# Kernel tuning notes

Measured on AMD Instinct MI355X. Metric: run time of the kernel, lower is better.

The kernel has to match this reference:

```python
import jax, jax.numpy as jnp
import numpy as np

B, S, D, H = 2, 2048, 1024, 16
HD = D // H  # 64


def setup_inputs() -> dict:
    key = jax.random.key(0)
    ks = jax.random.split(key, 12)
    scale = 1.0 / np.sqrt(D)
    inp = {
        "input_query": jax.random.normal(ks[0], (B, S, D), jnp.float32),
        "input_key": jax.random.normal(ks[1], (B, S, D), jnp.float32),
        "input_value": jax.random.normal(ks[2], (B, S, D), jnp.float32),
        "mask": jax.random.randint(ks[3], (B, 1, S), 0, 2, jnp.int32),
        # torch nn.Linear params: y = x @ W.T + b, W shape (out, in)
        "wq": jax.random.uniform(ks[4], (D, D), jnp.float32, -scale, scale),
        "bq": jax.random.uniform(ks[5], (D,), jnp.float32, -scale, scale),
        "wk": jax.random.uniform(ks[6], (D, D), jnp.float32, -scale, scale),
        "bk": jax.random.uniform(ks[7], (D,), jnp.float32, -scale, scale),
        "wv": jax.random.uniform(ks[8], (D, D), jnp.float32, -scale, scale),
        "bv": jax.random.uniform(ks[9], (D,), jnp.float32, -scale, scale),
        "wo": jax.random.uniform(ks[10], (D, D), jnp.float32, -scale, scale),
        "bo": jax.random.uniform(ks[11], (D,), jnp.float32, -scale, scale),
    }
    return inp


def _split_heads(x):
    # (B, S, D) -> (B, H, S, HD)
    return x.reshape(B, S, H, HD).transpose(0, 2, 1, 3)


def reference(input_query, input_key, input_value, mask, wq, bq, wk, bk, wv, bv, wo, bo):
    q = _split_heads(input_query @ wq.T + bq)
    k = _split_heads(input_key @ wk.T + bk)
    v = _split_heads(input_value @ wv.T + bv)

    # scaled dot-product attention (materializes [B,H,S,S] as the original does)
    scores = jnp.einsum("bhqd,bhkd->bhqk", q, k) / np.sqrt(HD).astype(np.float32)
    # mask: (B, 1, S) -> unsqueeze(1) -> (B, 1, 1, S); fill -1e9 where mask == 0
    m = mask[:, None, :, :]
    scores = jnp.where(m == 0, jnp.float32(-1e9), scores)
    p_attn = jax.nn.softmax(scores, axis=-1)  # dropout is identity (rate 0 / eval)

    out = jnp.einsum("bhqk,bhkd->bhqd", p_attn, v)
    out = out.transpose(0, 2, 1, 3).reshape(B, S, D)
    return out @ wo.T + bo
```

## Files before the change

kernel.cpp:

```cpp
#include <hip/hip_runtime.h>
#include <math.h>

#define BB 2
#define SS 2048
#define DD 1024
#define HH 16
#define HD 64

typedef short short8 __attribute__((ext_vector_type(8)));
typedef float floatx4 __attribute__((ext_vector_type(4)));
typedef float floatx16 __attribute__((ext_vector_type(16)));
typedef unsigned int uintx2 __attribute__((ext_vector_type(2)));

__device__ inline ushort f2bf_rne(float x) {
    union { float f; unsigned u; } v; v.f = x;
    unsigned r = v.u + 0x7FFFu + ((v.u >> 16) & 1u);
    return (ushort)(r >> 16);
}
__device__ inline unsigned cvt_pk_bf16(float lo, float hi) {
    unsigned r;
    asm("v_cvt_pk_bf16_f32 %0, %1, %2" : "=v"(r) : "v"(lo), "v"(hi));
    return r;
}
__device__ inline short8 mk_pf(uintx2 x, uintx2 y) {
    union { unsigned u[4]; short8 s; } t;
    t.u[0] = x[0]; t.u[1] = y[0]; t.u[2] = x[1]; t.u[3] = y[1];
    return t.s;
}

#define GLD16(gp, lp) __builtin_amdgcn_global_load_lds( \
    (const __attribute__((address_space(1))) void*)(gp), \
    (__attribute__((address_space(3))) void*)(lp), 16, 0, 0)

__global__ __launch_bounds__(256)
void convert_bf16(const float* __restrict__ xq, const float* __restrict__ xk,
                  const float* __restrict__ xv,
                  const float* __restrict__ wq, const float* __restrict__ wk,
                  const float* __restrict__ wv, const float* __restrict__ wo,
                  ushort* __restrict__ Xq, ushort* __restrict__ Xk,
                  ushort* __restrict__ Xv,
                  ushort* __restrict__ Wq, ushort* __restrict__ Wk,
                  ushort* __restrict__ Wv, ushort* __restrict__ Wo)
{
    const int z = blockIdx.z;
    const size_t i = ((size_t)blockIdx.x * 256 + threadIdx.x) * 8;

    const float* src;
    ushort* dst;
    size_t off;
    if (z < 3) {
        src = (z == 0) ? xq : (z == 1) ? xk : xv;
        dst = (z == 0) ? Xq : (z == 1) ? Xk : Xv;
        off = i;
    } else {
        const int seg = (int)(i >> 20);
        off = i & ((1u << 20) - 1);
        src = (seg == 0) ? wq : (seg == 1) ? wk : (seg == 2) ? wv : wo;
        dst = (seg == 0) ? Wq : (seg == 1) ? Wk : (seg == 2) ? Wv : Wo;
    }
    float x[8];
    *(float4*)&x[0] = *(const float4*)(src + off);
    *(float4*)&x[4] = *(const float4*)(src + off + 4);
    short8 h8;
#pragma unroll
    for (int j = 0; j < 8; ++j) h8[j] = (short)f2bf_rne(x[j]);
    *(short8*)&dst[off] = h8;
}

__global__ __launch_bounds__(256, 3)
void qkv_gemm(const ushort* __restrict__ Xq, const ushort* __restrict__ Xk,
              const ushort* __restrict__ Xv,
              const ushort* __restrict__ Wq, const ushort* __restrict__ Wk,
              const ushort* __restrict__ Wv,
              const float* __restrict__ bq, const float* __restrict__ bk,
              const float* __restrict__ bv, const int* __restrict__ mask,
              ushort* __restrict__ Qo, ushort* __restrict__ Ko,
              ushort* __restrict__ Vo, float qscale)
{
    __shared__ __align__(16) ushort Alds[128][32];
    __shared__ __align__(16) ushort Blds[128][32];

    const int z   = blockIdx.z;
    const int tid = threadIdx.x;

    const ushort* X    = (z == 0) ? Xq : (z == 1) ? Xk : Xv;
    const ushort* W    = (z == 0) ? Wq : (z == 1) ? Wk : Wv;
    const float*  bias = (z == 0) ? bq : (z == 1) ? bk : bv;
    const float   osc  = (z == 0) ? qscale : 1.0f;

    const int lane = tid & 63;
    const int wave = tid >> 6;
    const int wr = wave >> 1;
    const int wc = wave & 1;
    const int lt = lane & 15;
    const int lq = lane >> 4;
    const int m0 = blockIdx.y * 128;
    const int n0 = blockIdx.x * 128;

    floatx4 acc[4][4];
#pragma unroll
    for (int mi = 0; mi < 4; ++mi)
#pragma unroll
        for (int ni = 0; ni < 4; ++ni) acc[mi][ni] = (floatx4)0.0f;

    const int srow = tid >> 2;
    const int sc   = (tid & 3) << 3;
    const ushort* gA0 = X + (size_t)(m0 + srow) * DD + sc;
    const ushort* gA1 = X + (size_t)(m0 + 64 + srow) * DD + sc;
    const ushort* gB0 = W + (size_t)(n0 + srow) * DD + sc;
    const ushort* gB1 = W + (size_t)(n0 + 64 + srow) * DD + sc;

    for (int k0 = 0; k0 < DD; k0 += 32) {
        __syncthreads();
        GLD16(gA0 + k0, &Alds[srow][sc]);
        GLD16(gA1 + k0, &Alds[64 + srow][sc]);
        GLD16(gB0 + k0, &Blds[srow][sc]);
        GLD16(gB1 + k0, &Blds[64 + srow][sc]);
        __syncthreads();

        short8 af[4], bf_[4];
#pragma unroll
        for (int mi = 0; mi < 4; ++mi)
            af[mi] = *(const short8*)&Alds[wr * 64 + mi * 16 + lt][lq * 8];
#pragma unroll
        for (int ni = 0; ni < 4; ++ni)
            bf_[ni] = *(const short8*)&Blds[wc * 64 + ni * 16 + lt][lq * 8];

#pragma unroll
        for (int mi = 0; mi < 4; ++mi)
#pragma unroll
            for (int ni = 0; ni < 4; ++ni)
                acc[mi][ni] = __builtin_amdgcn_mfma_f32_16x16x32_bf16(af[mi], bf_[ni], acc[mi][ni], 0, 0, 0);
    }

    float bbv[4];
#pragma unroll
    for (int ni = 0; ni < 4; ++ni) bbv[ni] = bias[n0 + wc * 64 + ni * 16 + lt];

    if (z == 2) {
#pragma unroll
        for (int mi = 0; mi < 4; ++mi) {
            const int mb  = m0 + wr * 64 + mi * 16 + lq * 4;
            const int bb_ = mb >> 11;
            const int s   = mb & (SS - 1);
            const int4 mm = *(const int4*)(mask + bb_ * SS + s);
            const float mf0 = (float)mm.x, mf1 = (float)mm.y;
            const float mf2 = (float)mm.z, mf3 = (float)mm.w;
#pragma unroll
            for (int ni = 0; ni < 4; ++ni) {
                const int n = n0 + wc * 64 + ni * 16 + lt;
                const int h = n >> 6;
                ushort4 pack;
                pack.x = f2bf_rne((acc[mi][ni][0] + bbv[ni]) * mf0);
                pack.y = f2bf_rne((acc[mi][ni][1] + bbv[ni]) * mf1);
                pack.z = f2bf_rne((acc[mi][ni][2] + bbv[ni]) * mf2);
                pack.w = f2bf_rne((acc[mi][ni][3] + bbv[ni]) * mf3);
                *(ushort4*)&Vo[(size_t)((bb_ * HH + h) * HD + (n & 63)) * SS + s] = pack;
            }
        }
    } else {
        ushort* C = z ? Ko : Qo;
#pragma unroll
        for (int mi = 0; mi < 4; ++mi) {
            const int mb  = m0 + wr * 64 + mi * 16 + lq * 4;
            const int bb_ = mb >> 11;
            const int s   = mb & (SS - 1);
            float mf[4] = {1.0f, 1.0f, 1.0f, 1.0f};
            if (z == 1) {
                const int4 mm = *(const int4*)(mask + bb_ * SS + s);
                mf[0] = (float)mm.x; mf[1] = (float)mm.y;
                mf[2] = (float)mm.z; mf[3] = (float)mm.w;
            }
#pragma unroll
            for (int ni = 0; ni < 4; ++ni) {
                const int n = n0 + wc * 64 + ni * 16 + lt;
                const int h = n >> 6;
#pragma unroll
                for (int r = 0; r < 4; ++r) {
                    C[(size_t)((bb_ * HH + h) * SS + (s + r)) * HD + (n & 63)] =
                        f2bf_rne((acc[mi][ni][r] + bbv[ni]) * osc * mf[r]);
                }
            }
        }
    }
}

#define LDV 68

__global__ __launch_bounds__(512, 4)
void attn_mfma(const ushort* __restrict__ Qb, const ushort* __restrict__ Kb,
               const ushort* __restrict__ Vt, const int* __restrict__ mask,
               ushort* __restrict__ Ob)
{
    __shared__ __align__(16) ushort KVlds[4][64][LDV];
    __shared__ int Wsum[8];

    const int tid  = threadIdx.x;
    const int lane = tid & 63;
    const int wave = tid >> 6;
    const int ll   = lane & 31;
    const int hi   = lane >> 5;
    const int qh   = wave & 3;
    const int ks   = wave >> 2;

    const int bid    = blockIdx.x;
    const int xcd    = bid & 7;
    const int slot   = bid >> 3;
    const int bhloc  = slot >> 4;
    const int qi     = slot & 15;
    const int bh     = xcd * 4 + bhloc;
    const int b      = bh >> 4;
    const int q0     = qi * 128;

    const size_t sbase = (size_t)bh * SS * HD;
    const size_t vbase = (size_t)bh * HD * SS;

    {
        const int4 ma = *(const int4*)(mask + b * SS + tid * 4);
        int s = ma.x + ma.y + ma.z + ma.w;
#pragma unroll
        for (int w = 32; w >= 1; w >>= 1) s += __shfl_xor(s, w);
        if (lane == 0) Wsum[wave] = s;
    }

    short8 ones;
#pragma unroll
    for (int j = 0; j < 8; ++j) ones[j] = (short)0x3F80;

    short8 qf[4];
    {
        const size_t qrow = sbase + (size_t)(q0 + qh * 32 + ll) * HD;
#pragma unroll
        for (int dc = 0; dc < 4; ++dc)
            qf[dc] = *(const short8*)(Qb + qrow + dc * 16 + hi * 8);
    }

    floatx16 oacc[2];
    oacc[0] = (floatx16)0.0f;
    oacc[1] = (floatx16)0.0f;
    floatx16 lacc = (floatx16)0.0f;

    const int srow = tid >> 3;
    const int sp8  = (tid & 7) << 3;

    short8 kr, vr;

    {
        kr = *(const short8*)(Kb + sbase + (size_t)srow * HD + sp8);
        vr = *(const short8*)(Vt + vbase + (size_t)srow * SS + sp8);
        *(short8*)&KVlds[0][srow][sp8] = kr;
        *(short8*)&KVlds[2][srow][sp8] = vr;
    }

    const int NT = SS / 64;
    for (int kt = 0; kt < NT; ++kt) {
        const int cur = kt & 1;
        __syncthreads();

        if (kt + 1 < NT) {
            const int k0n = (kt + 1) * 64;
            kr = *(const short8*)(Kb + sbase + (size_t)(k0n + srow) * HD + sp8);
            vr = *(const short8*)(Vt + vbase + (size_t)srow * SS + k0n + sp8);
        }

        short8 kf[4];
#pragma unroll
        for (int dc = 0; dc < 4; ++dc)
            kf[dc] = *(const short8*)&KVlds[cur][ks * 32 + ll][dc * 16 + hi * 8];

        floatx16 sacc = (floatx16)0.0f;
#pragma unroll
        for (int dc = 0; dc < 4; ++dc)
            sacc = __builtin_amdgcn_mfma_f32_32x32x16_bf16(kf[dc], qf[dc], sacc, 0, 0, 0);

        float p[16];
#pragma unroll
        for (int r = 0; r < 16; ++r) p[r] = __builtin_amdgcn_exp2f(sacc[r]);

        const unsigned pk_a = cvt_pk_bf16(p[0],  p[1]);
        const unsigned pk_b = cvt_pk_bf16(p[2],  p[3]);
        const unsigned pk_c = cvt_pk_bf16(p[4],  p[5]);
        const unsigned pk_d = cvt_pk_bf16(p[6],  p[7]);
        const unsigned pk_e = cvt_pk_bf16(p[8],  p[9]);
        const unsigned pk_f = cvt_pk_bf16(p[10], p[11]);
        const unsigned pk_g = cvt_pk_bf16(p[12], p[13]);
        const unsigned pk_h = cvt_pk_bf16(p[14], p[15]);
        const uintx2 s1 = __builtin_amdgcn_permlane32_swap(pk_a, pk_c, false, false);
        const uintx2 s2 = __builtin_amdgcn_permlane32_swap(pk_b, pk_d, false, false);
        const uintx2 s3 = __builtin_amdgcn_permlane32_swap(pk_e, pk_g, false, false);
        const uintx2 s4 = __builtin_amdgcn_permlane32_swap(pk_f, pk_h, false, false);
        const short8 pf0 = mk_pf(s1, s2);
        const short8 pf1 = mk_pf(s3, s4);

        lacc = __builtin_amdgcn_mfma_f32_32x32x16_bf16(pf0, ones, lacc, 0, 0, 0);
        lacc = __builtin_amdgcn_mfma_f32_32x32x16_bf16(pf1, ones, lacc, 0, 0, 0);

#pragma unroll
        for (int dn = 0; dn < 2; ++dn) {
            const short8 vf0 = *(const short8*)&KVlds[2 + cur][dn * 32 + ll][ks * 32 + hi * 8];
            const short8 vf1 = *(const short8*)&KVlds[2 + cur][dn * 32 + ll][ks * 32 + 16 + hi * 8];
            oacc[dn] = __builtin_amdgcn_mfma_f32_32x32x16_bf16(pf0, vf0, oacc[dn], 0, 0, 0);
            oacc[dn] = __builtin_amdgcn_mfma_f32_32x32x16_bf16(pf1, vf1, oacc[dn], 0, 0, 0);
        }

        if (kt + 1 < NT) {
            const int nxt = cur ^ 1;
            *(short8*)&KVlds[nxt][srow][sp8]     = kr;
            *(short8*)&KVlds[2 + nxt][srow][sp8] = vr;
        }
    }

    float* Cmb = (float*)&KVlds[0][0][0];
#pragma unroll
    for (int ph = 0; ph < 2; ++ph) {
        __syncthreads();
        if (ks == 1 && (qh >> 1) == ph) {
            const int sl = qh & 1;
#pragma unroll
            for (int dn = 0; dn < 2; ++dn)
#pragma unroll
                for (int r = 0; r < 16; ++r)
                    Cmb[((sl * 2 + dn) * 16 + r) * 64 + lane] = oacc[dn][r];
#pragma unroll
            for (int r = 0; r < 16; ++r)
                Cmb[4096 + (sl * 16 + r) * 64 + lane] = lacc[r];
        }
        __syncthreads();
        if (ks == 0 && (qh >> 1) == ph) {
            const int sl = qh & 1;
#pragma unroll
            for (int dn = 0; dn < 2; ++dn)
#pragma unroll
                for (int r = 0; r < 16; ++r)
                    oacc[dn][r] += Cmb[((sl * 2 + dn) * 16 + r) * 64 + lane];
#pragma unroll
            for (int r = 0; r < 16; ++r)
                lacc[r] += Cmb[4096 + (sl * 16 + r) * 64 + lane];
        }
    }

    if (ks == 0) {
        const int h = bh & 15;
        const float nmf = (float)(SS - (Wsum[0] + Wsum[1] + Wsum[2] + Wsum[3]
                                      + Wsum[4] + Wsum[5] + Wsum[6] + Wsum[7]));
        float linv[16];
#pragma unroll
        for (int r = 0; r < 16; ++r) linv[r] = 1.0f / (lacc[r] - nmf);
#pragma unroll
        for (int dn = 0; dn < 2; ++dn)
#pragma unroll
            for (int r = 0; r < 16; ++r) {
                const int q = q0 + qh * 32 + (r & 3) + 8 * (r >> 2) + 4 * hi;
                Ob[(size_t)(b * SS + q) * DD + h * HD + dn * 32 + ll] =
                    f2bf_rne(oacc[dn][r] * linv[r]);
            }
    }
}

__global__ __launch_bounds__(256, 3)
void o_gemm(const ushort* __restrict__ A, const ushort* __restrict__ B,
            const float* __restrict__ bias, float* __restrict__ out)
{
    __shared__ __align__(16) ushort sA[128][32];
    __shared__ __align__(16) ushort sB[128][32];

    const int tid  = threadIdx.x;
    const int lane = tid & 63;
    const int wave = tid >> 6;
    const int wr = wave >> 1;
    const int wc = wave & 1;
    const int lt = lane & 15;
    const int lq = lane >> 4;
    const int m0 = blockIdx.y * 128;
    const int n0 = blockIdx.x * 128;

    floatx4 acc[4][4];
#pragma unroll
    for (int mi = 0; mi < 4; ++mi)
#pragma unroll
        for (int ni = 0; ni < 4; ++ni) acc[mi][ni] = (floatx4)0.0f;

    const int srow = tid >> 2;
    const int sc   = (tid & 3) << 3;
    const ushort* gA0 = A + (size_t)(m0 + srow) * DD + sc;
    const ushort* gA1 = A + (size_t)(m0 + 64 + srow) * DD + sc;
    const ushort* gB0 = B + (size_t)(n0 + srow) * DD + sc;
    const ushort* gB1 = B + (size_t)(n0 + 64 + srow) * DD + sc;

    for (int k0 = 0; k0 < DD; k0 += 32) {
        __syncthreads();
        GLD16(gA0 + k0, &sA[srow][sc]);
        GLD16(gA1 + k0, &sA[64 + srow][sc]);
        GLD16(gB0 + k0, &sB[srow][sc]);
        GLD16(gB1 + k0, &sB[64 + srow][sc]);
        __syncthreads();

        short8 af[4], bf_[4];
#pragma unroll
        for (int mi = 0; mi < 4; ++mi)
            af[mi] = *(const short8*)&sA[wr * 64 + mi * 16 + lt][lq * 8];
#pragma unroll
        for (int ni = 0; ni < 4; ++ni)
            bf_[ni] = *(const short8*)&sB[wc * 64 + ni * 16 + lt][lq * 8];

#pragma unroll
        for (int mi = 0; mi < 4; ++mi)
#pragma unroll
            for (int ni = 0; ni < 4; ++ni)
                acc[mi][ni] = __builtin_amdgcn_mfma_f32_16x16x32_bf16(af[mi], bf_[ni], acc[mi][ni], 0, 0, 0);
    }

#pragma unroll
    for (int mi = 0; mi < 4; ++mi)
#pragma unroll
        for (int ni = 0; ni < 4; ++ni) {
            const int n = n0 + wc * 64 + ni * 16 + lt;
            const float bb = bias[n];
#pragma unroll
            for (int r = 0; r < 4; ++r) {
                const int m = m0 + wr * 64 + mi * 16 + lq * 4 + r;
                out[(size_t)m * DD + n] = acc[mi][ni][r] + bb;
            }
        }
}

extern "C" void kernel_launch(void* const* d_in, const int* in_sizes, int n_in,
                              void* d_out, int out_size, void* d_ws, size_t ws_size,
                              hipStream_t stream) {
    const float* xq   = (const float*)d_in[0];
    const float* xk   = (const float*)d_in[1];
    const float* xv   = (const float*)d_in[2];
    const int*   mask = (const int*)d_in[3];
    const float* wq   = (const float*)d_in[4];
    const float* bq   = (const float*)d_in[5];
    const float* wk   = (const float*)d_in[6];
    const float* bk   = (const float*)d_in[7];
    const float* wv   = (const float*)d_in[8];
    const float* bv   = (const float*)d_in[9];
    const float* wo   = (const float*)d_in[10];
    const float* bo   = (const float*)d_in[11];
    float* out = (float*)d_out;

    const size_t n = (size_t)BB * SS * DD;
    const size_t w1 = (size_t)DD * DD;

    ushort* Xqb = (ushort*)d_ws;
    ushort* Xkb = Xqb + n;
    ushort* Xvb = Xkb + n;
    ushort* Kb  = Xvb + n;
    ushort* Vt  = Kb + n;
    ushort* Wob = Vt + n;
    ushort* Ob  = Xqb;

    ushort* Qb  = (ushort*)out;
    ushort* Wqb = Qb + n;
    ushort* Wkb = Wqb + w1;
    ushort* Wvb = Wkb + w1;

    const float qscale = 0.125f * 1.44269504088896340736f;

    dim3 gc(2048, 1, 4);
    convert_bf16<<<gc, 256, 0, stream>>>(xq, xk, xv, wq, wk, wv, wo,
                                         Xqb, Xkb, Xvb, Wqb, Wkb, Wvb, Wob);

    dim3 g1(DD / 128, (BB * SS) / 128, 3);
    qkv_gemm<<<g1, 256, 0, stream>>>(Xqb, Xkb, Xvb, Wqb, Wkb, Wvb,
                                     bq, bk, bv, mask, Qb, Kb, Vt, qscale);

    attn_mfma<<<dim3(512), 512, 0, stream>>>(Qb, Kb, Vt, mask, Ob);

    dim3 g2(DD / 128, (BB * SS) / 128);
    o_gemm<<<g2, 256, 0, stream>>>(Ob, Wob, bo, out);
}
```

Baseline: 227.9 us.

## Stage QKV epilogue via LDS, shrink attention and output GEMM tiles

The QKV GEMM epilogue now writes results into a shared-memory staging buffer and then emits 16-byte coalesced stores to Q/K and transposed V, replacing scattered 2-byte and 8-byte stores. The attention kernel moves from 512-thread blocks over 128 queries to 256-thread blocks over 64 queries, doubling the grid. It also adds s_setprio around the MFMA bursts and simplifies the cross-wave reduction. The output GEMM uses 128x64 tiles so twice as many blocks cover the CUs, at the cost of less B-tile reuse and extra syncs in the epilogue.

```diff
diff --git a/kernel.cpp b/kernel.cpp
--- a/kernel.cpp
+++ b/kernel.cpp
@@ -77,8 +77,10 @@
               ushort* __restrict__ Qo, ushort* __restrict__ Ko,
               ushort* __restrict__ Vo, float qscale)
 {
-    __shared__ __align__(16) ushort Alds[128][32];
-    __shared__ __align__(16) ushort Blds[128][32];
+    __shared__ __align__(16) ushort SMEM[8704];
+#define ALDS(r, c) SMEM[(r) * 32 + (c)]
+#define BLDS(r, c) SMEM[4096 + (r) * 32 + (c)]
+#define EPI(r, c)  SMEM[(r) * 136 + (c)]
 
     const int z   = blockIdx.z;
     const int tid = threadIdx.x;
@@ -112,19 +114,19 @@
 
     for (int k0 = 0; k0 < DD; k0 += 32) {
         __syncthreads();
-        GLD16(gA0 + k0, &Alds[srow][sc]);
-        GLD16(gA1 + k0, &Alds[64 + srow][sc]);
-        GLD16(gB0 + k0, &Blds[srow][sc]);
-        GLD16(gB1 + k0, &Blds[64 + srow][sc]);
+        GLD16(gA0 + k0, &ALDS(srow, sc));
+        GLD16(gA1 + k0, &ALDS(64 + srow, sc));
+        GLD16(gB0 + k0, &BLDS(srow, sc));
+        GLD16(gB1 + k0, &BLDS(64 + srow, sc));
         __syncthreads();
 
         short8 af[4], bf_[4];
 #pragma unroll
         for (int mi = 0; mi < 4; ++mi)
-            af[mi] = *(const short8*)&Alds[wr * 64 + mi * 16 + lt][lq * 8];
+            af[mi] = *(const short8*)&ALDS(wr * 64 + mi * 16 + lt, lq * 8);
 #pragma unroll
         for (int ni = 0; ni < 4; ++ni)
-            bf_[ni] = *(const short8*)&Blds[wc * 64 + ni * 16 + lt][lq * 8];
+            bf_[ni] = *(const short8*)&BLDS(wc * 64 + ni * 16 + lt, lq * 8);
 
 #pragma unroll
         for (int mi = 0; mi < 4; ++mi)
@@ -139,85 +141,118 @@
 
     if (z == 2) {
 #pragma unroll
-        for (int mi = 0; mi < 4; ++mi) {
-            const int mb  = m0 + wr * 64 + mi * 16 + lq * 4;
-            const int bb_ = mb >> 11;
-            const int s   = mb & (SS - 1);
-            const int4 mm = *(const int4*)(mask + bb_ * SS + s);
-            const float mf0 = (float)mm.x, mf1 = (float)mm.y;
-            const float mf2 = (float)mm.z, mf3 = (float)mm.w;
-#pragma unroll
-            for (int ni = 0; ni < 4; ++ni) {
-                const int n = n0 + wc * 64 + ni * 16 + lt;
+        for (int half = 0; half < 2; ++half) {
+            __syncthreads();
+            if (wc == half) {
+#pragma unroll
+                for (int mi = 0; mi < 4; ++mi) {
+                    const int mb  = m0 + wr * 64 + mi * 16 + lq * 4;
+                    const int bb_ = mb >> 11;
+                    const int s   = mb & (SS - 1);
+                    const int4 mm = *(const int4*)(mask + bb_ * SS + s);
+                    const float mf[4] = {(float)mm.x, (float)mm.y, (float)mm.z, (float)mm.w};
+#pragma unroll
+                    for (int ni = 0; ni < 4; ++ni)
+#pragma unroll
+                        for (int r = 0; r < 4; ++r)
+                            EPI(ni * 16 + lt, wr * 64 + mi * 16 + lq * 4 + r) =
+                                f2bf_rne((acc[mi][ni][r] + bbv[ni]) * mf[r]);
+                }
+            }
+            __syncthreads();
+            const int b_ = m0 >> 11;
+            const int sB = m0 & (SS - 1);
+#pragma unroll
+            for (int u = 0; u < 4; ++u) {
+                const int idx = u * 256 + tid;
+                const int row = idx >> 4;
+                const int sg  = (idx & 15) << 3;
+                const short8 v = *(const short8*)&EPI(row, sg);
+                const int n = n0 + half * 64 + row;
                 const int h = n >> 6;
-                ushort4 pack;
-                pack.x = f2bf_rne((acc[mi][ni][0] + bbv[ni]) * mf0);
-                pack.y = f2bf_rne((acc[mi][ni][1] + bbv[ni]) * mf1);
-                pack.z = f2bf_rne((acc[mi][ni][2] + bbv[ni]) * mf2);
-                pack.w = f2bf_rne((acc[mi][ni][3] + bbv[ni]) * mf3);
-                *(ushort4*)&Vo[(size_t)((bb_ * HH + h) * HD + (n & 63)) * SS + s] = pack;
+                *(short8*)&Vo[((size_t)(b_ * HH + h) * HD + (n & 63)) * SS + sB + sg] = v;
             }
         }
     } else {
         ushort* C = z ? Ko : Qo;
 #pragma unroll
-        for (int mi = 0; mi < 4; ++mi) {
-            const int mb  = m0 + wr * 64 + mi * 16 + lq * 4;
-            const int bb_ = mb >> 11;
-            const int s   = mb & (SS - 1);
-            float mf[4] = {1.0f, 1.0f, 1.0f, 1.0f};
-            if (z == 1) {
-                const int4 mm = *(const int4*)(mask + bb_ * SS + s);
-                mf[0] = (float)mm.x; mf[1] = (float)mm.y;
-                mf[2] = (float)mm.z; mf[3] = (float)mm.w;
-            }
-#pragma unroll
-            for (int ni = 0; ni < 4; ++ni) {
-                const int n = n0 + wc * 64 + ni * 16 + lt;
-                const int h = n >> 6;
-#pragma unroll
-                for (int r = 0; r < 4; ++r) {
-                    C[(size_t)((bb_ * HH + h) * SS + (s + r)) * HD + (n & 63)] =
-                        f2bf_rne((acc[mi][ni][r] + bbv[ni]) * osc * mf[r]);
+        for (int half = 0; half < 2; ++half) {
+            __syncthreads();
+            if (wr == half) {
+#pragma unroll
+                for (int mi = 0; mi < 4; ++mi) {
+                    const int mb  = m0 + half * 64 + mi * 16 + lq * 4;
+                    const int bb_ = mb >> 11;
+                    const int s   = mb & (SS - 1);
+                    float mf[4] = {1.0f, 1.0f, 1.0f, 1.0f};
+                    if (z == 1) {
+                        const int4 mm = *(const int4*)(mask + bb_ * SS + s);
+                        mf[0] = (float)mm.x; mf[1] = (float)mm.y;
+                        mf[2] = (float)mm.z; mf[3] = (float)mm.w;
+                    }
+#pragma unroll
+                    for (int ni = 0; ni < 4; ++ni)
+#pragma unroll
+                        for (int r = 0; r < 4; ++r)
+                            EPI(mi * 16 + lq * 4 + r, wc * 64 + ni * 16 + lt) =
+                                f2bf_rne((acc[mi][ni][r] + bbv[ni]) * osc * mf[r]);
                 }
             }
+            __syncthreads();
+#pragma unroll
+            for (int u = 0; u < 4; ++u) {
+                const int idx = u * 256 + tid;
+                const int row = idx >> 4;
+                const int cg  = (idx & 15) << 3;
+                const short8 v = *(const short8*)&EPI(row, cg);
+                const int m = m0 + half * 64 + row;
+                const int n = n0 + cg;
+                const int h = n >> 6;
+                const int b_ = m >> 11;
+                const int s  = m & (SS - 1);
+                *(short8*)&C[((size_t)(b_ * HH + h) * SS + s) * HD + (n & 63)] = v;
+            }
         }
     }
+#undef ALDS
+#undef BLDS
+#undef EPI
 }
 
 #define LDV 68
 
-__global__ __launch_bounds__(512, 4)
+__global__ __launch_bounds__(256, 4)
 void attn_mfma(const ushort* __restrict__ Qb, const ushort* __restrict__ Kb,
                const ushort* __restrict__ Vt, const int* __restrict__ mask,
                ushort* __restrict__ Ob)
 {
     __shared__ __align__(16) ushort KVlds[4][64][LDV];
-    __shared__ int Wsum[8];
+    __shared__ int Wsum[4];
 
     const int tid  = threadIdx.x;
     const int lane = tid & 63;
     const int wave = tid >> 6;
     const int ll   = lane & 31;
     const int hi   = lane >> 5;
-    const int qh   = wave & 3;
-    const int ks   = wave >> 2;
+    const int qh   = wave & 1;
+    const int ks   = wave >> 1;
 
     const int bid    = blockIdx.x;
     const int xcd    = bid & 7;
     const int slot   = bid >> 3;
-    const int bhloc  = slot >> 4;
-    const int qi     = slot & 15;
+    const int bhloc  = slot >> 5;
+    const int qi     = slot & 31;
     const int bh     = xcd * 4 + bhloc;
     const int b      = bh >> 4;
-    const int q0     = qi * 128;
+    const int q0     = qi * 64;
 
     const size_t sbase = (size_t)bh * SS * HD;
     const size_t vbase = (size_t)bh * HD * SS;
 
     {
-        const int4 ma = *(const int4*)(mask + b * SS + tid * 4);
-        int s = ma.x + ma.y + ma.z + ma.w;
+        const int4 ma = *(const int4*)(mask + b * SS + tid * 8);
+        const int4 mb = *(const int4*)(mask + b * SS + tid * 8 + 4);
+        int s = ma.x + ma.y + ma.z + ma.w + mb.x + mb.y + mb.z + mb.w;
 #pragma unroll
         for (int w = 32; w >= 1; w >>= 1) s += __shfl_xor(s, w);
         if (lane == 0) Wsum[wave] = s;
@@ -240,16 +275,22 @@
     oacc[1] = (floatx16)0.0f;
     floatx16 lacc = (floatx16)0.0f;
 
-    const int srow = tid >> 3;
-    const int sp8  = (tid & 7) << 3;
-
-    short8 kr, vr;
+    const int srow = tid >> 2;
+    const int sp16 = (tid & 3) << 4;
+
+    short8 kr0, kr1, vr0, vr1;
 
     {
-        kr = *(const short8*)(Kb + sbase + (size_t)srow * HD + sp8);
-        vr = *(const short8*)(Vt + vbase + (size_t)srow * SS + sp8);
-        *(short8*)&KVlds[0][srow][sp8] = kr;
-        *(short8*)&KVlds[2][srow][sp8] = vr;
+        const size_t koff = sbase + (size_t)srow * HD + sp16;
+        kr0 = *(const short8*)(Kb + koff);
+        kr1 = *(const short8*)(Kb + koff + 8);
+        const size_t voff = vbase + (size_t)srow * SS + sp16;
+        vr0 = *(const short8*)(Vt + voff);
+        vr1 = *(const short8*)(Vt + voff + 8);
+        *(short8*)&KVlds[0][srow][sp16]     = kr0;
+        *(short8*)&KVlds[0][srow][sp16 + 8] = kr1;
+        *(short8*)&KVlds[2][srow][sp16]     = vr0;
+        *(short8*)&KVlds[2][srow][sp16 + 8] = vr1;
     }
 
     const int NT = SS / 64;
@@ -259,8 +300,12 @@
 
         if (kt + 1 < NT) {
             const int k0n = (kt + 1) * 64;
-            kr = *(const short8*)(Kb + sbase + (size_t)(k0n + srow) * HD + sp8);
-            vr = *(const short8*)(Vt + vbase + (size_t)srow * SS + k0n + sp8);
+            const size_t koff = sbase + (size_t)(k0n + srow) * HD + sp16;
+            kr0 = *(const short8*)(Kb + koff);
+            kr1 = *(const short8*)(Kb + koff + 8);
+            const size_t voff = vbase + (size_t)srow * SS + k0n + sp16;
+            vr0 = *(const short8*)(Vt + voff);
+            vr1 = *(const short8*)(Vt + voff + 8);
         }
 
         short8 kf[4];
@@ -269,9 +314,11 @@
             kf[dc] = *(const short8*)&KVlds[cur][ks * 32 + ll][dc * 16 + hi * 8];
 
         floatx16 sacc = (floatx16)0.0f;
+        __builtin_amdgcn_s_setprio(1);
 #pragma unroll
         for (int dc = 0; dc < 4; ++dc)
             sacc = __builtin_amdgcn_mfma_f32_32x32x16_bf16(kf[dc], qf[dc], sacc, 0, 0, 0);
+        __builtin_amdgcn_s_setprio(0);
 
         float p[16];
 #pragma unroll
@@ -292,9 +339,9 @@
         const short8 pf0 = mk_pf(s1, s2);
         const short8 pf1 = mk_pf(s3, s4);
 
+        __builtin_amdgcn_s_setprio(1);
         lacc = __builtin_amdgcn_mfma_f32_32x32x16_bf16(pf0, ones, lacc, 0, 0, 0);
         lacc = __builtin_amdgcn_mfma_f32_32x32x16_bf16(pf1, ones, lacc, 0, 0, 0);
-
 #pragma unroll
         for (int dn = 0; dn < 2; ++dn) {
             const short8 vf0 = *(const short8*)&KVlds[2 + cur][dn * 32 + ll][ks * 32 + hi * 8];
@@ -302,47 +349,42 @@
             oacc[dn] = __builtin_amdgcn_mfma_f32_32x32x16_bf16(pf0, vf0, oacc[dn], 0, 0, 0);
             oacc[dn] = __builtin_amdgcn_mfma_f32_32x32x16_bf16(pf1, vf1, oacc[dn], 0, 0, 0);
         }
+        __builtin_amdgcn_s_setprio(0);
 
         if (kt + 1 < NT) {
             const int nxt = cur ^ 1;
-            *(short8*)&KVlds[nxt][srow][sp8]     = kr;
-            *(short8*)&KVlds[2 + nxt][srow][sp8] = vr;
+            *(short8*)&KVlds[nxt][srow][sp16]     = kr0;
+            *(short8*)&KVlds[nxt][srow][sp16 + 8] = kr1;
+            *(short8*)&KVlds[2 + nxt][srow][sp16]     = vr0;
+            *(short8*)&KVlds[2 + nxt][srow][sp16 + 8] = vr1;
         }
     }
 
     float* Cmb = (float*)&KVlds[0][0][0];
-#pragma unroll
-    for (int ph = 0; ph < 2; ++ph) {
-        __syncthreads();
-        if (ks == 1 && (qh >> 1) == ph) {
-            const int sl = qh & 1;
-#pragma unroll
-            for (int dn = 0; dn < 2; ++dn)
-#pragma unroll
-                for (int r = 0; r < 16; ++r)
-                    Cmb[((sl * 2 + dn) * 16 + r) * 64 + lane] = oacc[dn][r];
+    __syncthreads();
+    if (ks == 1) {
+#pragma unroll
+        for (int dn = 0; dn < 2; ++dn)
 #pragma unroll
             for (int r = 0; r < 16; ++r)
-                Cmb[4096 + (sl * 16 + r) * 64 + lane] = lacc[r];
-        }
-        __syncthreads();
-        if (ks == 0 && (qh >> 1) == ph) {
-            const int sl = qh & 1;
-#pragma unroll
-            for (int dn = 0; dn < 2; ++dn)
-#pragma unroll
-                for (int r = 0; r < 16; ++r)
-                    oacc[dn][r] += Cmb[((sl * 2 + dn) * 16 + r) * 64 + lane];
+                Cmb[((qh * 2 + dn) * 16 + r) * 64 + lane] = oacc[dn][r];
+#pragma unroll
+        for (int r = 0; r < 16; ++r)
+            Cmb[4096 + (qh * 16 + r) * 64 + lane] = lacc[r];
+    }
+    __syncthreads();
+    if (ks == 0) {
+#pragma unroll
+        for (int dn = 0; dn < 2; ++dn)
 #pragma unroll
             for (int r = 0; r < 16; ++r)
-                lacc[r] += Cmb[4096 + (sl * 16 + r) * 64 + lane];
-        }
-    }
-
-    if (ks == 0) {
+                oacc[dn][r] += Cmb[((qh * 2 + dn) * 16 + r) * 64 + lane];
+#pragma unroll
+        for (int r = 0; r < 16; ++r)
+            lacc[r] += Cmb[4096 + (qh * 16 + r) * 64 + lane];
+
         const int h = bh & 15;
-        const float nmf = (float)(SS - (Wsum[0] + Wsum[1] + Wsum[2] + Wsum[3]
-                                      + Wsum[4] + Wsum[5] + Wsum[6] + Wsum[7]));
+        const float nmf = (float)(SS - (Wsum[0] + Wsum[1] + Wsum[2] + Wsum[3]));
         float linv[16];
 #pragma unroll
         for (int r = 0; r < 16; ++r) linv[r] = 1.0f / (lacc[r] - nmf);
@@ -362,7 +404,7 @@
             const float* __restrict__ bias, float* __restrict__ out)
 {
     __shared__ __align__(16) ushort sA[128][32];
-    __shared__ __align__(16) ushort sB[128][32];
+    __shared__ __align__(16) ushort sB[64][32];
 
     const int tid  = threadIdx.x;
     const int lane = tid & 63;
@@ -372,49 +414,47 @@
     const int lt = lane & 15;
     const int lq = lane >> 4;
     const int m0 = blockIdx.y * 128;
-    const int n0 = blockIdx.x * 128;
-
-    floatx4 acc[4][4];
+    const int n0 = blockIdx.x * 64;
+
+    floatx4 acc[4][2];
 #pragma unroll
     for (int mi = 0; mi < 4; ++mi)
 #pragma unroll
-        for (int ni = 0; ni < 4; ++ni) acc[mi][ni] = (floatx4)0.0f;
+        for (int ni = 0; ni < 2; ++ni) acc[mi][ni] = (floatx4)0.0f;
 
     const int srow = tid >> 2;
     const int sc   = (tid & 3) << 3;
     const ushort* gA0 = A + (size_t)(m0 + srow) * DD + sc;
     const ushort* gA1 = A + (size_t)(m0 + 64 + srow) * DD + sc;
     const ushort* gB0 = B + (size_t)(n0 + srow) * DD + sc;
-    const ushort* gB1 = B + (size_t)(n0 + 64 + srow) * DD + sc;
 
     for (int k0 = 0; k0 < DD; k0 += 32) {
         __syncthreads();
         GLD16(gA0 + k0, &sA[srow][sc]);
         GLD16(gA1 + k0, &sA[64 + srow][sc]);
         GLD16(gB0 + k0, &sB[srow][sc]);
-        GLD16(gB1 + k0, &sB[64 + srow][sc]);
         __syncthreads();
 
-        short8 af[4], bf_[4];
+        short8 af[4], bf_[2];
 #pragma unroll
         for (int mi = 0; mi < 4; ++mi)
             af[mi] = *(const short8*)&sA[wr * 64 + mi * 16 + lt][lq * 8];
 #pragma unroll
-        for (int ni = 0; ni < 4; ++ni)
-            bf_[ni] = *(const short8*)&sB[wc * 64 + ni * 16 + lt][lq * 8];
+        for (int ni = 0; ni < 2; ++ni)
+            bf_[ni] = *(const short8*)&sB[wc * 32 + ni * 16 + lt][lq * 8];
 
 #pragma unroll
         for (int mi = 0; mi < 4; ++mi)
 #pragma unroll
-            for (int ni = 0; ni < 4; ++ni)
+            for (int ni = 0; ni < 2; ++ni)
                 acc[mi][ni] = __builtin_amdgcn_mfma_f32_16x16x32_bf16(af[mi], bf_[ni], acc[mi][ni], 0, 0, 0);
     }
 
 #pragma unroll
     for (int mi = 0; mi < 4; ++mi)
 #pragma unroll
-        for (int ni = 0; ni < 4; ++ni) {
-            const int n = n0 + wc * 64 + ni * 16 + lt;
+        for (int ni = 0; ni < 2; ++ni) {
+            const int n = n0 + wc * 32 + ni * 16 + lt;
             const float bb = bias[n];
 #pragma unroll
             for (int r = 0; r < 4; ++r) {
@@ -467,8 +507,8 @@
     qkv_gemm<<<g1, 256, 0, stream>>>(Xqb, Xkb, Xvb, Wqb, Wkb, Wvb,
                                      bq, bk, bv, mask, Qb, Kb, Vt, qscale);
 
-    attn_mfma<<<dim3(512), 512, 0, stream>>>(Qb, Kb, Vt, mask, Ob);
-
-    dim3 g2(DD / 128, (BB * SS) / 128);
+    attn_mfma<<<dim3(1024), 256, 0, stream>>>(Qb, Kb, Vt, mask, Ob);
+
+    dim3 g2(DD / 64, (BB * SS) / 128);
     o_gemm<<<g2, 256, 0, stream>>>(Ob, Wob, bo, out);
 }
```

Measured after the change: 219.4 us. 3.7% less time.

## Fuse fp32-to-bf16 conversion into GEMM loads, remap blocks, add MFMA priorities

Applied to the files above, without the earlier changes.

Removes the separate conversion kernel. The QKV and output GEMMs now load fp32 activations and weights directly, convert them to bf16 in registers, and write them to LDS. Both GEMMs move to 1D grids with XCD-aware block remapping, and the output GEMM switches to 128x64 tiles so it launches more blocks. The attention loop wraps its MFMA sections in s_setprio. This saves a full read/write pass over the inputs and weights, but the GEMMs now read twice the bytes per tile through plain register loads instead of direct-to-LDS loads, and weights are re-converted by every block.

```diff
diff --git a/kernel.cpp b/kernel.cpp
--- a/kernel.cpp
+++ b/kernel.cpp
@@ -22,6 +22,14 @@
     asm("v_cvt_pk_bf16_f32 %0, %1, %2" : "=v"(r) : "v"(lo), "v"(hi));
     return r;
 }
+__device__ inline short8 cvt8(float4 lo, float4 hi) {
+    union { unsigned u[4]; short8 s; } t;
+    t.u[0] = cvt_pk_bf16(lo.x, lo.y);
+    t.u[1] = cvt_pk_bf16(lo.z, lo.w);
+    t.u[2] = cvt_pk_bf16(hi.x, hi.y);
+    t.u[3] = cvt_pk_bf16(hi.z, hi.w);
+    return t.s;
+}
 __device__ inline short8 mk_pf(uintx2 x, uintx2 y) {
     union { unsigned u[4]; short8 s; } t;
     t.u[0] = x[0]; t.u[1] = y[0]; t.u[2] = x[1]; t.u[3] = y[1];
@@ -32,46 +40,11 @@
     (const __attribute__((address_space(1))) void*)(gp), \
     (__attribute__((address_space(3))) void*)(lp), 16, 0, 0)
 
-__global__ __launch_bounds__(256)
-void convert_bf16(const float* __restrict__ xq, const float* __restrict__ xk,
-                  const float* __restrict__ xv,
-                  const float* __restrict__ wq, const float* __restrict__ wk,
-                  const float* __restrict__ wv, const float* __restrict__ wo,
-                  ushort* __restrict__ Xq, ushort* __restrict__ Xk,
-                  ushort* __restrict__ Xv,
-                  ushort* __restrict__ Wq, ushort* __restrict__ Wk,
-                  ushort* __restrict__ Wv, ushort* __restrict__ Wo)
-{
-    const int z = blockIdx.z;
-    const size_t i = ((size_t)blockIdx.x * 256 + threadIdx.x) * 8;
-
-    const float* src;
-    ushort* dst;
-    size_t off;
-    if (z < 3) {
-        src = (z == 0) ? xq : (z == 1) ? xk : xv;
-        dst = (z == 0) ? Xq : (z == 1) ? Xk : Xv;
-        off = i;
-    } else {
-        const int seg = (int)(i >> 20);
-        off = i & ((1u << 20) - 1);
-        src = (seg == 0) ? wq : (seg == 1) ? wk : (seg == 2) ? wv : wo;
-        dst = (seg == 0) ? Wq : (seg == 1) ? Wk : (seg == 2) ? Wv : Wo;
-    }
-    float x[8];
-    *(float4*)&x[0] = *(const float4*)(src + off);
-    *(float4*)&x[4] = *(const float4*)(src + off + 4);
-    short8 h8;
-#pragma unroll
-    for (int j = 0; j < 8; ++j) h8[j] = (short)f2bf_rne(x[j]);
-    *(short8*)&dst[off] = h8;
-}
-
 __global__ __launch_bounds__(256, 3)
-void qkv_gemm(const ushort* __restrict__ Xq, const ushort* __restrict__ Xk,
-              const ushort* __restrict__ Xv,
-              const ushort* __restrict__ Wq, const ushort* __restrict__ Wk,
-              const ushort* __restrict__ Wv,
+void qkv_gemm(const float* __restrict__ Xq, const float* __restrict__ Xk,
+              const float* __restrict__ Xv,
+              const float* __restrict__ Wq, const float* __restrict__ Wk,
+              const float* __restrict__ Wv,
               const float* __restrict__ bq, const float* __restrict__ bk,
               const float* __restrict__ bv, const int* __restrict__ mask,
               ushort* __restrict__ Qo, ushort* __restrict__ Ko,
@@ -80,13 +53,18 @@
     __shared__ __align__(16) ushort Alds[128][32];
     __shared__ __align__(16) ushort Blds[128][32];
 
-    const int z   = blockIdx.z;
     const int tid = threadIdx.x;
 
-    const ushort* X    = (z == 0) ? Xq : (z == 1) ? Xk : Xv;
-    const ushort* W    = (z == 0) ? Wq : (z == 1) ? Wk : Wv;
-    const float*  bias = (z == 0) ? bq : (z == 1) ? bk : bv;
-    const float   osc  = (z == 0) ? qscale : 1.0f;
+    const int wg  = (blockIdx.x & 7) * 96 + (blockIdx.x >> 3);
+    const int z   = wg >> 8;
+    const int rem = wg & 255;
+    const int m0  = (rem >> 3) * 128;
+    const int n0  = (rem & 7) * 128;
+
+    const float* X    = (z == 0) ? Xq : (z == 1) ? Xk : Xv;
+    const float* W    = (z == 0) ? Wq : (z == 1) ? Wk : Wv;
+    const float* bias = (z == 0) ? bq : (z == 1) ? bk : bv;
+    const float  osc  = (z == 0) ? qscale : 1.0f;
 
     const int lane = tid & 63;
     const int wave = tid >> 6;
@@ -94,8 +72,6 @@
     const int wc = wave & 1;
     const int lt = lane & 15;
     const int lq = lane >> 4;
-    const int m0 = blockIdx.y * 128;
-    const int n0 = blockIdx.x * 128;
 
     floatx4 acc[4][4];
 #pragma unroll
@@ -103,19 +79,26 @@
 #pragma unroll
         for (int ni = 0; ni < 4; ++ni) acc[mi][ni] = (floatx4)0.0f;
 
-    const int srow = tid >> 2;
-    const int sc   = (tid & 3) << 3;
-    const ushort* gA0 = X + (size_t)(m0 + srow) * DD + sc;
-    const ushort* gA1 = X + (size_t)(m0 + 64 + srow) * DD + sc;
-    const ushort* gB0 = W + (size_t)(n0 + srow) * DD + sc;
-    const ushort* gB1 = W + (size_t)(n0 + 64 + srow) * DD + sc;
+    const int srow = tid >> 1;
+    const int sks  = (tid & 1) << 4;
+    const float* gA = X + (size_t)(m0 + srow) * DD + sks;
+    const float* gB = W + (size_t)(n0 + srow) * DD + sks;
 
     for (int k0 = 0; k0 < DD; k0 += 32) {
-        __syncthreads();
-        GLD16(gA0 + k0, &Alds[srow][sc]);
-        GLD16(gA1 + k0, &Alds[64 + srow][sc]);
-        GLD16(gB0 + k0, &Blds[srow][sc]);
-        GLD16(gB1 + k0, &Blds[64 + srow][sc]);
+        const float4 a0 = *(const float4*)(gA + k0);
+        const float4 a1 = *(const float4*)(gA + k0 + 4);
+        const float4 a2 = *(const float4*)(gA + k0 + 8);
+        const float4 a3 = *(const float4*)(gA + k0 + 12);
+        const float4 b0 = *(const float4*)(gB + k0);
+        const float4 b1 = *(const float4*)(gB + k0 + 4);
+        const float4 b2 = *(const float4*)(gB + k0 + 8);
+        const float4 b3 = *(const float4*)(gB + k0 + 12);
+
+        __syncthreads();
+        *(short8*)&Alds[srow][sks]     = cvt8(a0, a1);
+        *(short8*)&Alds[srow][sks + 8] = cvt8(a2, a3);
+        *(short8*)&Blds[srow][sks]     = cvt8(b0, b1);
+        *(short8*)&Blds[srow][sks + 8] = cvt8(b2, b3);
         __syncthreads();
 
         short8 af[4], bf_[4];
@@ -269,9 +252,11 @@
             kf[dc] = *(const short8*)&KVlds[cur][ks * 32 + ll][dc * 16 + hi * 8];
 
         floatx16 sacc = (floatx16)0.0f;
+        __builtin_amdgcn_s_setprio(1);
 #pragma unroll
         for (int dc = 0; dc < 4; ++dc)
             sacc = __builtin_amdgcn_mfma_f32_32x32x16_bf16(kf[dc], qf[dc], sacc, 0, 0, 0);
+        __builtin_amdgcn_s_setprio(0);
 
         float p[16];
 #pragma unroll
@@ -292,9 +277,9 @@
         const short8 pf0 = mk_pf(s1, s2);
         const short8 pf1 = mk_pf(s3, s4);
 
+        __builtin_amdgcn_s_setprio(1);
         lacc = __builtin_amdgcn_mfma_f32_32x32x16_bf16(pf0, ones, lacc, 0, 0, 0);
         lacc = __builtin_amdgcn_mfma_f32_32x32x16_bf16(pf1, ones, lacc, 0, 0, 0);
-
 #pragma unroll
         for (int dn = 0; dn < 2; ++dn) {
             const short8 vf0 = *(const short8*)&KVlds[2 + cur][dn * 32 + ll][ks * 32 + hi * 8];
@@ -302,6 +287,7 @@
             oacc[dn] = __builtin_amdgcn_mfma_f32_32x32x16_bf16(pf0, vf0, oacc[dn], 0, 0, 0);
             oacc[dn] = __builtin_amdgcn_mfma_f32_32x32x16_bf16(pf1, vf1, oacc[dn], 0, 0, 0);
         }
+        __builtin_amdgcn_s_setprio(0);
 
         if (kt + 1 < NT) {
             const int nxt = cur ^ 1;
@@ -358,11 +344,11 @@
 }
 
 __global__ __launch_bounds__(256, 3)
-void o_gemm(const ushort* __restrict__ A, const ushort* __restrict__ B,
+void o_gemm(const ushort* __restrict__ A, const float* __restrict__ B,
             const float* __restrict__ bias, float* __restrict__ out)
 {
     __shared__ __align__(16) ushort sA[128][32];
-    __shared__ __align__(16) ushort sB[128][32];
+    __shared__ __align__(16) ushort sB[64][32];
 
     const int tid  = threadIdx.x;
     const int lane = tid & 63;
@@ -371,50 +357,52 @@
     const int wc = wave & 1;
     const int lt = lane & 15;
     const int lq = lane >> 4;
-    const int m0 = blockIdx.y * 128;
-    const int n0 = blockIdx.x * 128;
-
-    floatx4 acc[4][4];
+
+    const int wg = (blockIdx.x & 7) * 64 + (blockIdx.x >> 3);
+    const int m0 = (wg >> 4) * 128;
+    const int n0 = (wg & 15) * 64;
+
+    floatx4 acc[4][2];
 #pragma unroll
     for (int mi = 0; mi < 4; ++mi)
 #pragma unroll
-        for (int ni = 0; ni < 4; ++ni) acc[mi][ni] = (floatx4)0.0f;
+        for (int ni = 0; ni < 2; ++ni) acc[mi][ni] = (floatx4)0.0f;
 
     const int srow = tid >> 2;
     const int sc   = (tid & 3) << 3;
     const ushort* gA0 = A + (size_t)(m0 + srow) * DD + sc;
     const ushort* gA1 = A + (size_t)(m0 + 64 + srow) * DD + sc;
-    const ushort* gB0 = B + (size_t)(n0 + srow) * DD + sc;
-    const ushort* gB1 = B + (size_t)(n0 + 64 + srow) * DD + sc;
+    const float*  gB  = B + (size_t)(n0 + srow) * DD + sc;
 
     for (int k0 = 0; k0 < DD; k0 += 32) {
+        const float4 b0 = *(const float4*)(gB + k0);
+        const float4 b1 = *(const float4*)(gB + k0 + 4);
         __syncthreads();
         GLD16(gA0 + k0, &sA[srow][sc]);
         GLD16(gA1 + k0, &sA[64 + srow][sc]);
-        GLD16(gB0 + k0, &sB[srow][sc]);
-        GLD16(gB1 + k0, &sB[64 + srow][sc]);
-        __syncthreads();
-
-        short8 af[4], bf_[4];
+        *(short8*)&sB[srow][sc] = cvt8(b0, b1);
+        __syncthreads();
+
+        short8 af[4], bf_[2];
 #pragma unroll
         for (int mi = 0; mi < 4; ++mi)
             af[mi] = *(const short8*)&sA[wr * 64 + mi * 16 + lt][lq * 8];
 #pragma unroll
-        for (int ni = 0; ni < 4; ++ni)
-            bf_[ni] = *(const short8*)&sB[wc * 64 + ni * 16 + lt][lq * 8];
+        for (int ni = 0; ni < 2; ++ni)
+            bf_[ni] = *(const short8*)&sB[wc * 32 + ni * 16 + lt][lq * 8];
 
 #pragma unroll
         for (int mi = 0; mi < 4; ++mi)
 #pragma unroll
-            for (int ni = 0; ni < 4; ++ni)
+            for (int ni = 0; ni < 2; ++ni)
                 acc[mi][ni] = __builtin_amdgcn_mfma_f32_16x16x32_bf16(af[mi], bf_[ni], acc[mi][ni], 0, 0, 0);
     }
 
 #pragma unroll
     for (int mi = 0; mi < 4; ++mi)
 #pragma unroll
-        for (int ni = 0; ni < 4; ++ni) {
-            const int n = n0 + wc * 64 + ni * 16 + lt;
+        for (int ni = 0; ni < 2; ++ni) {
+            const int n = n0 + wc * 32 + ni * 16 + lt;
             const float bb = bias[n];
 #pragma unroll
             for (int r = 0; r < 4; ++r) {
@@ -442,33 +430,19 @@
     float* out = (float*)d_out;
 
     const size_t n = (size_t)BB * SS * DD;
-    const size_t w1 = (size_t)DD * DD;
-
-    ushort* Xqb = (ushort*)d_ws;
-    ushort* Xkb = Xqb + n;
-    ushort* Xvb = Xkb + n;
-    ushort* Kb  = Xvb + n;
-    ushort* Vt  = Kb + n;
-    ushort* Wob = Vt + n;
-    ushort* Ob  = Xqb;
-
-    ushort* Qb  = (ushort*)out;
-    ushort* Wqb = Qb + n;
-    ushort* Wkb = Wqb + w1;
-    ushort* Wvb = Wkb + w1;
+
+    ushort* Kb = (ushort*)d_ws;
+    ushort* Vt = Kb + n;
+    ushort* Ob = Vt + n;
+
+    ushort* Qb = (ushort*)out;
 
     const float qscale = 0.125f * 1.44269504088896340736f;
 
-    dim3 gc(2048, 1, 4);
-    convert_bf16<<<gc, 256, 0, stream>>>(xq, xk, xv, wq, wk, wv, wo,
-                                         Xqb, Xkb, Xvb, Wqb, Wkb, Wvb, Wob);
-
-    dim3 g1(DD / 128, (BB * SS) / 128, 3);
-    qkv_gemm<<<g1, 256, 0, stream>>>(Xqb, Xkb, Xvb, Wqb, Wkb, Wvb,
-                                     bq, bk, bv, mask, Qb, Kb, Vt, qscale);
+    qkv_gemm<<<dim3(768), 256, 0, stream>>>(xq, xk, xv, wq, wk, wv,
+                                            bq, bk, bv, mask, Qb, Kb, Vt, qscale);
 
     attn_mfma<<<dim3(512), 512, 0, stream>>>(Qb, Kb, Vt, mask, Ob);
 
-    dim3 g2(DD / 128, (BB * SS) / 128);
-    o_gemm<<<g2, 256, 0, stream>>>(Ob, Wob, bo, out);
-}
+    o_gemm<<<dim3(512), 256, 0, stream>>>(Ob, wo, bo, out);
+}
```

New measurement: 249.2 us. 9.4% more time.
